# Kernel optimization log

Measured on AMD Instinct MI355X. Metric: run time of the kernel, lower is better.

The kernel has to match this reference:

```python
import jax, jax.numpy as jnp
import numpy as np

N, D, H, C, E, ED, HID = 50000, 160, 5, 32, 800000, 16, 512
EPS = 1e-5  # torch LayerNorm default
NEG_SLOPE = 0.2  # GATv2Conv default negative_slope


def layer_norm(x, g, b):
    mu = x.mean(-1, keepdims=True)
    var = x.var(-1, keepdims=True)  # biased, matches torch LayerNorm
    return (x - mu) * jax.lax.rsqrt(var + EPS) * g + b


def setup_inputs() -> dict:
    key = jax.random.key(0)
    ks = jax.random.split(key, 12)
    p = lambda k, shape: jax.random.normal(k, shape, jnp.float32) * 0.05
    z = lambda *s: jnp.zeros(s, jnp.float32)
    o = lambda *s: jnp.ones(s, jnp.float32)
    return {
        "x": jax.random.normal(ks[0], (N, D), jnp.float32),
        "edge_index": jax.random.randint(ks[1], (2, E), 0, N),
        "edge_attr": jax.random.normal(ks[2], (E, ED), jnp.float32),
        "u": jax.random.normal(ks[3], (1024, 64), jnp.float32),
        "batch": jax.random.randint(ks[4], (N,), 0, 1024),
        # GATv2Conv params (lin_l, lin_r, lin_edge, att, bias)
        "Wl": p(ks[5], (D, H * C)), "bl": z(H * C),
        "Wr": p(ks[6], (D, H * C)), "br": z(H * C),
        "We": p(ks[7], (ED, H * C)),
        "att": p(ks[8], (H, C)),
        "b_gat": z(H * C),
        # norm1
        "g1": o(D), "b1": z(D),
        # output MLP: Linear(D,HID) -> SELU -> LayerNorm(HID) -> Linear(HID,D)
        "W_m1": p(ks[9], (D, HID)), "b_m1": z(HID),
        "g_m": o(HID), "b_m": z(HID),
        "W_m2": p(ks[10], (HID, D)), "b_m2": z(D),
        # norm2
        "g2": o(D), "b2": z(D),
    }


def reference(x, edge_index, edge_attr, u, batch, Wl, bl, Wr, br, We, att, b_gat,
              g1, b1, W_m1, b_m1, g_m, b_m, W_m2, b_m2, g2, b2):
    src, dst = edge_index[0], edge_index[1]  # messages flow src -> dst
    xl = (x @ Wl + bl).reshape(N, H, C)      # source projection
    xr = (x @ Wr + br).reshape(N, H, C)      # target projection
    ea = (edge_attr @ We).reshape(E, H, C)
    # GATv2 scoring: att . leaky_relu(x_l[j] + x_r[i] + e_ij)
    e = jax.nn.leaky_relu(xl[src] + xr[dst] + ea, NEG_SLOPE)   # [E,H,C]
    score = jnp.einsum('ehc,hc->eh', e, att)                   # [E,H]
    # segment softmax over incoming edges of each target node
    mx = jax.ops.segment_max(score, dst, num_segments=N)       # [N,H]
    ex = jnp.exp(score - mx[dst])
    denom = jax.ops.segment_sum(ex, dst, num_segments=N)
    alpha = ex / denom[dst]                                    # [E,H]
    agg = jax.ops.segment_sum(alpha[:, :, None] * xl[src], dst, num_segments=N)
    attn = agg.reshape(N, H * C) + b_gat                       # concat heads
    # residual + norm, MLP, residual + norm (dropout=0)
    out = layer_norm(x + attn, g1, b1)
    h = layer_norm(jax.nn.selu(out @ W_m1 + b_m1), g_m, b_m)
    mlp = h @ W_m2 + b_m2
    return layer_norm(out + mlp, g2, b2)
```

## Files before the change

### kernel.cpp

```cpp
#include <hip/hip_runtime.h>
#include <math.h>

#define N_NODES 50000
#define D 160
#define H 5
#define C 32
#define HC 160
#define E_EDGES 800000
#define ED 16
#define HID 512
#define EPS 1e-5f
#define NEG_SLOPE 0.2f

typedef __attribute__((ext_vector_type(8))) short bf16x8;
typedef __attribute__((ext_vector_type(4))) float f32x4;
typedef __attribute__((ext_vector_type(4))) short short4v;

__device__ inline float bf2f(short s) {
  unsigned u = ((unsigned)(unsigned short)s) << 16;
  return __builtin_bit_cast(float, u);
}
__device__ inline short f2bf(float f) {
  unsigned u = __builtin_bit_cast(unsigned, f);
  u = u + 0x7fffu + ((u >> 16) & 1u);
  return (short)(u >> 16);
}
__device__ inline float selu_f(float v) {
  return 1.0507009873554805f * (v > 0.f ? v : 1.6732632423543772f * (__expf(v) - 1.f));
}

__global__ void prep_weights(const float* __restrict__ Wl, const float* __restrict__ Wr,
                             const float* __restrict__ Wm1, const float* __restrict__ Wm2,
                             const float* __restrict__ We,
                             short* __restrict__ WlT, short* __restrict__ WrT,
                             short* __restrict__ W1T, short* __restrict__ W2T,
                             short* __restrict__ WeTp) {
  int i = blockIdx.x * blockDim.x + threadIdx.x;
  if (i < 25600) { int n = i / 160, k = i % 160; WlT[n*160 + k] = f2bf(Wl[k*160 + n]); return; }
  i -= 25600;
  if (i < 25600) { int n = i / 160, k = i % 160; WrT[n*160 + k] = f2bf(Wr[k*160 + n]); return; }
  i -= 25600;
  if (i < 81920) { int n = i / 160, k = i % 160; W1T[n*160 + k] = f2bf(Wm1[k*512 + n]); return; }
  i -= 81920;
  if (i < 81920) { int n = i / 512, k = i % 512; W2T[n*512 + k] = f2bf(Wm2[k*160 + n]); return; }
  i -= 81920;
  if (i < 5120) { int col = i / 32, k = i % 32;
    WeTp[col*32 + k] = (k < ED) ? f2bf(We[k*160 + col]) : (short)0; }
}

__global__ void convert_x(const float* __restrict__ x, short* __restrict__ xb) {
  int i = blockIdx.x * blockDim.x + threadIdx.x;
  if (i < N_NODES * D / 8) {
    const float4* s = (const float4*)(x + (size_t)i * 8);
    float4 a = s[0], b = s[1];
    bf16x8 o;
    o[0] = f2bf(a.x); o[1] = f2bf(a.y); o[2] = f2bf(a.z); o[3] = f2bf(a.w);
    o[4] = f2bf(b.x); o[5] = f2bf(b.y); o[6] = f2bf(b.z); o[7] = f2bf(b.w);
    *(bf16x8*)(xb + (size_t)i * 8) = o;
  }
}

__global__ __launch_bounds__(256) void proj_mfma(
    const short* __restrict__ xb, const short* __restrict__ WlT, const short* __restrict__ WrT,
    const float* __restrict__ bl, const float* __restrict__ br,
    short* __restrict__ xl, short* __restrict__ xr)
{
  __shared__ short As[64][40];
  int t = threadIdx.x;
  int wave = t >> 6, lane = t & 63;
  int lq = lane >> 4, lc = lane & 15;
  int row0 = blockIdx.x * 64;
  f32x4 accl[10] = {}, accr[10] = {};
  for (int kt = 0; kt < 5; ++kt) {
    int k0 = kt * 32;
    {
      int r = t >> 2, seg = t & 3;
      int gr = min(row0 + r, N_NODES - 1);
      bf16x8 v = *(const bf16x8*)&xb[(size_t)gr * 160 + k0 + seg * 8];
      *(bf16x8*)&As[r][seg * 8] = v;
    }
    __syncthreads();
    bf16x8 af = *(bf16x8*)&As[wave * 16 + lc][lq * 8];
#pragma unroll
    for (int ct = 0; ct < 10; ++ct) {
      int cc = ct * 16 + lc;
      bf16x8 bfl = *(const bf16x8*)&WlT[cc * 160 + k0 + lq * 8];
      accl[ct] = __builtin_amdgcn_mfma_f32_16x16x32_bf16(af, bfl, accl[ct], 0, 0, 0);
      bf16x8 bfr = *(const bf16x8*)&WrT[cc * 160 + k0 + lq * 8];
      accr[ct] = __builtin_amdgcn_mfma_f32_16x16x32_bf16(af, bfr, accr[ct], 0, 0, 0);
    }
    __syncthreads();
  }
#pragma unroll
  for (int ct = 0; ct < 10; ++ct) {
    int col = ct * 16 + lc;
    float bbl = bl[col], bbr = br[col];
#pragma unroll
    for (int rg = 0; rg < 4; ++rg) {
      int row = row0 + wave * 16 + lq * 4 + rg;
      if (row < N_NODES) {
        xl[(size_t)row * 160 + col] = f2bf(accl[ct][rg] + bbl);
        xr[(size_t)row * 160 + col] = f2bf(accr[ct][rg] + bbr);
      }
    }
  }
}

__global__ void count_kernel(const int* __restrict__ ei, int* __restrict__ cnt) {
  int e = blockIdx.x * blockDim.x + threadIdx.x;
  if (e < E_EDGES) atomicAdd(&cnt[ei[E_EDGES + e]], 1);
}

__global__ __launch_bounds__(1024) void scan_kernel(const int* __restrict__ cnt,
                                                    int* __restrict__ offs) {
  const int PER = (N_NODES + 1023) / 1024;
  int t = threadIdx.x;
  int start = t * PER;
  int sum = 0;
  for (int i = 0; i < PER; ++i) {
    int idx = start + i;
    if (idx < N_NODES) sum += cnt[idx];
  }
  int lane = t & 63, wid = t >> 6;
  int v = sum;
  for (int off = 1; off < 64; off <<= 1) {
    int u = __shfl_up(v, off, 64);
    if (lane >= off) v += u;
  }
  __shared__ int wsums[16];
  if (lane == 63) wsums[wid] = v;
  __syncthreads();
  if (wid == 0) {
    int w = (lane < 16) ? wsums[lane] : 0;
    for (int off = 1; off < 16; off <<= 1) {
      int u = __shfl_up(w, off, 64);
      if (lane >= off) w += u;
    }
    if (lane < 16) wsums[lane] = w;
  }
  __syncthreads();
  int excl = v - sum + (wid > 0 ? wsums[wid - 1] : 0);
  int run = excl;
  for (int i = 0; i < PER; ++i) {
    int idx = start + i;
    if (idx < N_NODES) { offs[idx] = run; run += cnt[idx]; }
  }
  if (t == 1023) offs[N_NODES] = run;
}

__global__ void scatter3(const int* __restrict__ ei, const float* __restrict__ eattr,
                         const int* __restrict__ offs, int* __restrict__ cursor,
                         int* __restrict__ srcm, short* __restrict__ eacsr) {
  int e = blockIdx.x * blockDim.x + threadIdx.x;
  if (e < E_EDGES) {
    int dst = ei[E_EDGES + e];
    int src = ei[e];
    int slot = atomicAdd(&cursor[dst], 1);
    int j = offs[dst] + slot;
    srcm[j] = src * 160;
    const float4* s = (const float4*)&eattr[(size_t)e * ED];
    float4 v0 = s[0], v1 = s[1], v2 = s[2], v3 = s[3];
    short* o = eacsr + (size_t)j * ED;
    short4v w0, w1, w2, w3;
    w0[0]=f2bf(v0.x); w0[1]=f2bf(v0.y); w0[2]=f2bf(v0.z); w0[3]=f2bf(v0.w);
    w1[0]=f2bf(v1.x); w1[1]=f2bf(v1.y); w1[2]=f2bf(v1.z); w1[3]=f2bf(v1.w);
    w2[0]=f2bf(v2.x); w2[1]=f2bf(v2.y); w2[2]=f2bf(v2.z); w2[3]=f2bf(v2.w);
    w3[0]=f2bf(v3.x); w3[1]=f2bf(v3.y); w3[2]=f2bf(v3.z); w3[3]=f2bf(v3.w);
    *(short4v*)(o + 0) = w0; *(short4v*)(o + 4) = w1;
    *(short4v*)(o + 8) = w2; *(short4v*)(o + 12) = w3;
  }
}

__global__ __launch_bounds__(256) void attn_fused(
    const short* __restrict__ eacsr, const int* __restrict__ srcm,
    const short* __restrict__ WeTp, const short* __restrict__ xl, const short* __restrict__ xr,
    const float* __restrict__ att, const float* __restrict__ x,
    const float* __restrict__ b_gat, const float* __restrict__ g1, const float* __restrict__ b1,
    const int* __restrict__ offs,
    float* __restrict__ outb, short* __restrict__ outb_bf)
{
  int t = threadIdx.x;
  int wave = t >> 6, lane = t & 63;
  int lq = lane >> 4, lc = lane & 15;
  int i = blockIdx.x * 4 + wave;
  int e0 = offs[i], e1 = offs[i + 1];

  float xrv[10], attv[10];
#pragma unroll
  for (int ct = 0; ct < 10; ++ct) {
    xrv[ct] = bf2f(xr[(size_t)i * 160 + ct * 16 + lc]);
    attv[ct] = att[ct * 16 + lc];
  }
  float aggc[10] = {};
  float den[5] = {};
  const f32x4 zero4 = {};

  for (int j0 = e0; j0 < e1; j0 += 16) {
    bf16x8 af = {};
    if (lq < 2) {
      int jr = min(j0 + lc, e1 - 1);
      af = *(const bf16x8*)&eacsr[(size_t)jr * ED + lq * 8];
    }
    f32x4 acc[10];
#pragma unroll
    for (int ct = 0; ct < 10; ++ct) {
      bf16x8 bfv = *(const bf16x8*)&WeTp[(ct * 16 + lc) * 32 + lq * 8];
      acc[ct] = __builtin_amdgcn_mfma_f32_16x16x32_bf16(af, bfv, zero4, 0, 0, 0);
    }
    int src[4]; bool ok[4];
#pragma unroll
    for (int rg = 0; rg < 4; ++rg) {
      int j = j0 + lq * 4 + rg;
      ok[rg] = (j < e1);
      src[rg] = srcm[min(j, e1 - 1)];
    }
    float xlv[10][4];
    float partial[5][4] = {};
#pragma unroll
    for (int ct = 0; ct < 10; ++ct) {
#pragma unroll
      for (int rg = 0; rg < 4; ++rg) {
        float v = bf2f(xl[src[rg] + ct * 16 + lc]);
        xlv[ct][rg] = v;
        float z = acc[ct][rg] + v + xrv[ct];
        z = fmaxf(z, NEG_SLOPE * z);
        partial[ct >> 1][rg] = fmaf(z, attv[ct], partial[ct >> 1][rg]);
      }
    }
#pragma unroll
    for (int hh = 0; hh < 5; ++hh) {
#pragma unroll
      for (int rg = 0; rg < 4; ++rg) {
        float p = partial[hh][rg];
        p += __shfl_xor(p, 1, 64);
        p += __shfl_xor(p, 2, 64);
        p += __shfl_xor(p, 4, 64);
        p += __shfl_xor(p, 8, 64);
        float ex = ok[rg] ? __expf(p) : 0.f;
        den[hh] += ex;
        partial[hh][rg] = ex;
      }
    }
#pragma unroll
    for (int ct = 0; ct < 10; ++ct)
#pragma unroll
      for (int rg = 0; rg < 4; ++rg)
        aggc[ct] = fmaf(partial[ct >> 1][rg], xlv[ct][rg], aggc[ct]);
  }
#pragma unroll
  for (int ct = 0; ct < 10; ++ct) {
    aggc[ct] += __shfl_xor(aggc[ct], 16, 64);
    aggc[ct] += __shfl_xor(aggc[ct], 32, 64);
  }
#pragma unroll
  for (int hh = 0; hh < 5; ++hh) {
    den[hh] += __shfl_xor(den[hh], 16, 64);
    den[hh] += __shfl_xor(den[hh], 32, 64);
  }
  float val[10];
  float s1 = 0.f, s2 = 0.f;
#pragma unroll
  for (int ct = 0; ct < 10; ++ct) {
    float d = den[ct >> 1];
    float attn = (d > 0.f) ? aggc[ct] / d : 0.f;
    float v = x[(size_t)i * 160 + ct * 16 + lc] + attn + b_gat[ct * 16 + lc];
    val[ct] = v;
    s1 += v; s2 += v * v;
  }
#pragma unroll
  for (int m = 1; m <= 8; m <<= 1) { s1 += __shfl_xor(s1, m, 64); s2 += __shfl_xor(s2, m, 64); }
  float mu = s1 * (1.f / 160.f);
  float var = s2 * (1.f / 160.f) - mu * mu;
  float rstd = rsqrtf(var + EPS);
  if (lq == 0) {
#pragma unroll
    for (int ct = 0; ct < 10; ++ct) {
      int col = ct * 16 + lc;
      float o = (val[ct] - mu) * rstd * g1[col] + b1[col];
      outb[(size_t)i * 160 + col] = o;
      outb_bf[(size_t)i * 160 + col] = f2bf(o);
    }
  }
}

__global__ __launch_bounds__(256) void mlp1_mfma(
    const short* __restrict__ ab, const short* __restrict__ W1T,
    const float* __restrict__ b1m, const float* __restrict__ gm, const float* __restrict__ bm,
    short* __restrict__ h)
{
  __shared__ short As[32][40];
  __shared__ float ps1[4][32], ps2[4][32];
  int t = threadIdx.x;
  int wave = t >> 6, lane = t & 63;
  int lq = lane >> 4, lc = lane & 15;
  int row0 = blockIdx.x * 32;
  f32x4 acc[2][8] = {};
  for (int kt = 0; kt < 5; ++kt) {
    int k0 = kt * 32;
    if (t < 128) {
      int r = t >> 2, seg = t & 3;
      int gr = min(row0 + r, N_NODES - 1);
      bf16x8 v = *(const bf16x8*)&ab[(size_t)gr * 160 + k0 + seg * 8];
      *(bf16x8*)&As[r][seg * 8] = v;
    }
    __syncthreads();
    bf16x8 af0 = *(bf16x8*)&As[lc][lq * 8];
    bf16x8 af1 = *(bf16x8*)&As[16 + lc][lq * 8];
#pragma unroll
    for (int ct = 0; ct < 8; ++ct) {
      int cc = wave * 128 + ct * 16 + lc;
      bf16x8 bfv = *(const bf16x8*)&W1T[cc * 160 + k0 + lq * 8];
      acc[0][ct] = __builtin_amdgcn_mfma_f32_16x16x32_bf16(af0, bfv, acc[0][ct], 0, 0, 0);
      acc[1][ct] = __builtin_amdgcn_mfma_f32_16x16x32_bf16(af1, bfv, acc[1][ct], 0, 0, 0);
    }
    __syncthreads();
  }
  float s1[2][4] = {}, s2[2][4] = {};
#pragma unroll
  for (int rt = 0; rt < 2; ++rt)
#pragma unroll
    for (int ct = 0; ct < 8; ++ct)
#pragma unroll
      for (int rg = 0; rg < 4; ++rg) {
        int cc = wave * 128 + ct * 16 + lc;
        float v = selu_f(acc[rt][ct][rg] + b1m[cc]);
        acc[rt][ct][rg] = v;
        s1[rt][rg] += v; s2[rt][rg] += v * v;
      }
#pragma unroll
  for (int m = 1; m <= 8; m <<= 1) {
#pragma unroll
    for (int rt = 0; rt < 2; ++rt)
#pragma unroll
      for (int rg = 0; rg < 4; ++rg) {
        s1[rt][rg] += __shfl_xor(s1[rt][rg], m, 64);
        s2[rt][rg] += __shfl_xor(s2[rt][rg], m, 64);
      }
  }
  if (lc == 0) {
#pragma unroll
    for (int rt = 0; rt < 2; ++rt)
#pragma unroll
      for (int rg = 0; rg < 4; ++rg) {
        ps1[wave][rt * 16 + lq * 4 + rg] = s1[rt][rg];
        ps2[wave][rt * 16 + lq * 4 + rg] = s2[rt][rg];
      }
  }
  __syncthreads();
  float mu[2][4], rstd[2][4];
#pragma unroll
  for (int rt = 0; rt < 2; ++rt)
#pragma unroll
    for (int rg = 0; rg < 4; ++rg) {
      int rl = rt * 16 + lq * 4 + rg;
      float a = ps1[0][rl] + ps1[1][rl] + ps1[2][rl] + ps1[3][rl];
      float b = ps2[0][rl] + ps2[1][rl] + ps2[2][rl] + ps2[3][rl];
      float m_ = a * (1.f / 512.f);
      float var = b * (1.f / 512.f) - m_ * m_;
      mu[rt][rg] = m_; rstd[rt][rg] = rsqrtf(var + EPS);
    }
#pragma unroll
  for (int rt = 0; rt < 2; ++rt)
#pragma unroll
    for (int ct = 0; ct < 8; ++ct)
#pragma unroll
      for (int rg = 0; rg < 4; ++rg) {
        int row = row0 + rt * 16 + lq * 4 + rg;
        int cc = wave * 128 + ct * 16 + lc;
        if (row < N_NODES)
          h[(size_t)row * 512 + cc] =
              f2bf((acc[rt][ct][rg] - mu[rt][rg]) * rstd[rt][rg] * gm[cc] + bm[cc]);
      }
}

__global__ __launch_bounds__(256) void mlp2_mfma(
    const short* __restrict__ hb, const short* __restrict__ W2T,
    const float* __restrict__ b2m, const float* __restrict__ outb,
    const float* __restrict__ g2, const float* __restrict__ b2,
    float* __restrict__ y)
{
  __shared__ short As[128][72];
  int t = threadIdx.x;
  int wave = t >> 6, lane = t & 63;
  int lq = lane >> 4, lc = lane & 15;
  int row0 = blockIdx.x * 128;
  f32x4 acc[2][10] = {};
  for (int kt = 0; kt < 8; ++kt) {
    int k0 = kt * 64;
    __syncthreads();
#pragma unroll
    for (int q = 0; q < 4; ++q) {
      int idx = t + 256 * q;
      int r = idx >> 3, seg = idx & 7;
      int gr = min(row0 + r, N_NODES - 1);
      *(bf16x8*)&As[r][seg * 8] = *(const bf16x8*)&hb[(size_t)gr * 512 + k0 + seg * 8];
    }
    __syncthreads();
#pragma unroll
    for (int ks = 0; ks < 2; ++ks) {
      bf16x8 af0 = *(bf16x8*)&As[wave * 32 + lc][ks * 32 + lq * 8];
      bf16x8 af1 = *(bf16x8*)&As[wave * 32 + 16 + lc][ks * 32 + lq * 8];
#pragma unroll
      for (int ct = 0; ct < 10; ++ct) {
        bf16x8 bfv = *(const bf16x8*)&W2T[(ct * 16 + lc) * 512 + k0 + ks * 32 + lq * 8];
        acc[0][ct] = __builtin_amdgcn_mfma_f32_16x16x32_bf16(af0, bfv, acc[0][ct], 0, 0, 0);
        acc[1][ct] = __builtin_amdgcn_mfma_f32_16x16x32_bf16(af1, bfv, acc[1][ct], 0, 0, 0);
      }
    }
  }
  float s1[2][4] = {}, s2[2][4] = {};
#pragma unroll
  for (int rt = 0; rt < 2; ++rt)
#pragma unroll
    for (int ct = 0; ct < 10; ++ct) {
      int col = ct * 16 + lc;
#pragma unroll
      for (int rg = 0; rg < 4; ++rg) {
        int rowl = min(row0 + wave * 32 + rt * 16 + lq * 4 + rg, N_NODES - 1);
        float v = acc[rt][ct][rg] + b2m[col] + outb[(size_t)rowl * 160 + col];
        acc[rt][ct][rg] = v;
        s1[rt][rg] += v; s2[rt][rg] += v * v;
      }
    }
#pragma unroll
  for (int m = 1; m <= 8; m <<= 1) {
#pragma unroll
    for (int rt = 0; rt < 2; ++rt)
#pragma unroll
      for (int rg = 0; rg < 4; ++rg) {
        s1[rt][rg] += __shfl_xor(s1[rt][rg], m, 64);
        s2[rt][rg] += __shfl_xor(s2[rt][rg], m, 64);
      }
  }
  float mu[2][4], rstd[2][4];
#pragma unroll
  for (int rt = 0; rt < 2; ++rt)
#pragma unroll
    for (int rg = 0; rg < 4; ++rg) {
      float m_ = s1[rt][rg] * (1.f / 160.f);
      float var = s2[rt][rg] * (1.f / 160.f) - m_ * m_;
      mu[rt][rg] = m_; rstd[rt][rg] = rsqrtf(var + EPS);
    }
#pragma unroll
  for (int rt = 0; rt < 2; ++rt)
#pragma unroll
    for (int ct = 0; ct < 10; ++ct) {
      int col = ct * 16 + lc;
#pragma unroll
      for (int rg = 0; rg < 4; ++rg) {
        int row = row0 + wave * 32 + rt * 16 + lq * 4 + rg;
        if (row < N_NODES)
          y[(size_t)row * 160 + col] = (acc[rt][ct][rg] - mu[rt][rg]) * rstd[rt][rg] * g2[col] + b2[col];
      }
    }
}

extern "C" void kernel_launch(void* const* d_in, const int* in_sizes, int n_in,
                              void* d_out, int out_size, void* d_ws, size_t ws_size,
                              hipStream_t stream) {
  const float* x     = (const float*)d_in[0];
  const int*   ei    = (const int*)d_in[1];
  const float* eattr = (const float*)d_in[2];
  const float* Wl    = (const float*)d_in[5];
  const float* bl    = (const float*)d_in[6];
  const float* Wr    = (const float*)d_in[7];
  const float* br    = (const float*)d_in[8];
  const float* We    = (const float*)d_in[9];
  const float* att   = (const float*)d_in[10];
  const float* bgat  = (const float*)d_in[11];
  const float* g1    = (const float*)d_in[12];
  const float* b1    = (const float*)d_in[13];
  const float* Wm1   = (const float*)d_in[14];
  const float* bm1   = (const float*)d_in[15];
  const float* gm    = (const float*)d_in[16];
  const float* bm    = (const float*)d_in[17];
  const float* Wm2   = (const float*)d_in[18];
  const float* bm2   = (const float*)d_in[19];
  const float* g2    = (const float*)d_in[20];
  const float* b2    = (const float*)d_in[21];
  float* y = (float*)d_out;

  char* p = (char*)d_ws;
  auto alloc = [&](size_t bytes) {
    void* q = p;
    p += (bytes + 255) & ~(size_t)255;
    return q;
  };
  short* xb      = (short*)alloc((size_t)N_NODES * 160 * 2);
  short* xlb     = (short*)alloc((size_t)N_NODES * 160 * 2);
  short* xrb     = (short*)alloc((size_t)N_NODES * 160 * 2);
  float* outb    = (float*)alloc((size_t)N_NODES * 160 * 4);
  short* outb_bf = (short*)alloc((size_t)N_NODES * 160 * 2);
  short* hb      = (short*)alloc((size_t)N_NODES * 512 * 2);
  short* eacsr   = (short*)alloc((size_t)E_EDGES * ED * 2);
  int*   srcm    = (int*)alloc((size_t)E_EDGES * 4);
  short* WlT     = (short*)alloc(160 * 160 * 2);
  short* WrT     = (short*)alloc(160 * 160 * 2);
  short* W1T     = (short*)alloc(512 * 160 * 2);
  short* W2T     = (short*)alloc(160 * 512 * 2);
  short* WeTp    = (short*)alloc(160 * 32 * 2);
  int*   cnt     = (int*)alloc((size_t)N_NODES * 4);
  int*   offs    = (int*)alloc((size_t)(N_NODES + 1) * 4);
  int*   cursor  = (int*)alloc((size_t)N_NODES * 4);

  hipMemsetAsync(cnt, 0, (size_t)N_NODES * 4, stream);
  hipMemsetAsync(cursor, 0, (size_t)N_NODES * 4, stream);

  prep_weights<<<(220160 + 255) / 256, 256, 0, stream>>>(Wl, Wr, Wm1, Wm2, We,
                                                         WlT, WrT, W1T, W2T, WeTp);
  convert_x<<<(N_NODES * 160 / 8 + 255) / 256, 256, 0, stream>>>(x, xb);
  count_kernel<<<(E_EDGES + 255) / 256, 256, 0, stream>>>(ei, cnt);
  scan_kernel<<<1, 1024, 0, stream>>>(cnt, offs);
  scatter3<<<(E_EDGES + 255) / 256, 256, 0, stream>>>(ei, eattr, offs, cursor, srcm, eacsr);
  proj_mfma<<<(N_NODES + 63) / 64, 256, 0, stream>>>(xb, WlT, WrT, bl, br, xlb, xrb);
  attn_fused<<<N_NODES / 4, 256, 0, stream>>>(eacsr, srcm, WeTp, xlb, xrb, att, x,
                                              bgat, g1, b1, offs, outb, outb_bf);
  mlp1_mfma<<<(N_NODES + 31) / 32, 256, 0, stream>>>(outb_bf, W1T, bm1, gm, bm, hb);
  mlp2_mfma<<<(N_NODES + 127) / 128, 256, 0, stream>>>(hb, W2T, bm2, outb, g2, b2, y);
}
```

Measured before the change: 783.3 us.

## Stage gathered source rows in LDS and parallelize CSR offset scan

Replaces the single-block prefix scan over node in-degrees with a three-kernel multi-block scan (per-block scan, block-sum scan, add offsets). In the attention kernel, each wave now cooperatively gathers the 16 source xl rows for an edge chunk with 16-byte vector loads into padded shared memory, instead of each lane doing scattered 2-byte global loads. The MFMA edge projection is split into two halves to cut register pressure. The change adds LDS use and two extra launches; the LDS writes and reads within a wave rely on wave-level execution order with no explicit barrier.

Result: faster. 677.2 us (-13.5%).

```diff
diff --git a/kernel.cpp b/kernel.cpp
--- a/kernel.cpp
+++ b/kernel.cpp
@@ -111,41 +111,55 @@
   if (e < E_EDGES) atomicAdd(&cnt[ei[E_EDGES + e]], 1);
 }
 
-__global__ __launch_bounds__(1024) void scan_kernel(const int* __restrict__ cnt,
-                                                    int* __restrict__ offs) {
-  const int PER = (N_NODES + 1023) / 1024;
-  int t = threadIdx.x;
-  int start = t * PER;
-  int sum = 0;
-  for (int i = 0; i < PER; ++i) {
-    int idx = start + i;
-    if (idx < N_NODES) sum += cnt[idx];
-  }
+__global__ __launch_bounds__(1024) void scanA(const int* __restrict__ cnt,
+                                              int* __restrict__ pinc, int* __restrict__ bsum) {
+  int b = blockIdx.x, t = threadIdx.x;
+  int i = b * 1024 + t;
+  int v = (i < N_NODES) ? cnt[i] : 0;
   int lane = t & 63, wid = t >> 6;
-  int v = sum;
+  int s = v;
+#pragma unroll
   for (int off = 1; off < 64; off <<= 1) {
-    int u = __shfl_up(v, off, 64);
-    if (lane >= off) v += u;
-  }
-  __shared__ int wsums[16];
-  if (lane == 63) wsums[wid] = v;
+    int u = __shfl_up(s, off, 64);
+    if (lane >= off) s += u;
+  }
+  __shared__ int ws[16];
+  if (lane == 63) ws[wid] = s;
   __syncthreads();
   if (wid == 0) {
-    int w = (lane < 16) ? wsums[lane] : 0;
+    int w = (lane < 16) ? ws[lane] : 0;
+#pragma unroll
     for (int off = 1; off < 16; off <<= 1) {
       int u = __shfl_up(w, off, 64);
       if (lane >= off) w += u;
     }
-    if (lane < 16) wsums[lane] = w;
+    if (lane < 16) ws[lane] = w;
   }
   __syncthreads();
-  int excl = v - sum + (wid > 0 ? wsums[wid - 1] : 0);
-  int run = excl;
-  for (int i = 0; i < PER; ++i) {
-    int idx = start + i;
-    if (idx < N_NODES) { offs[idx] = run; run += cnt[idx]; }
-  }
-  if (t == 1023) offs[N_NODES] = run;
+  int incl = s + (wid > 0 ? ws[wid - 1] : 0);
+  if (i < N_NODES) pinc[i] = incl;
+  if (t == 1023) bsum[b] = incl;
+}
+
+__global__ void scanB(const int* __restrict__ bsum, int* __restrict__ boff) {
+  int t = threadIdx.x;
+  int v = (t < 49) ? bsum[t] : 0;
+  int s = v;
+#pragma unroll
+  for (int off = 1; off < 64; off <<= 1) {
+    int u = __shfl_up(s, off, 64);
+    if (t >= off) s += u;
+  }
+  if (t < 49) boff[t] = s - v;
+}
+
+__global__ __launch_bounds__(1024) void scanC(const int* __restrict__ pinc,
+                                              const int* __restrict__ boff,
+                                              int* __restrict__ offs) {
+  int b = blockIdx.x, t = threadIdx.x;
+  int i = b * 1024 + t;
+  if (i < N_NODES) offs[i + 1] = pinc[i] + boff[b];
+  if (i == 0) offs[0] = 0;
 }
 
 __global__ void scatter3(const int* __restrict__ ei, const float* __restrict__ eattr,
@@ -179,52 +193,68 @@
     const int* __restrict__ offs,
     float* __restrict__ outb, short* __restrict__ outb_bf)
 {
+  __shared__ short xt[4][16][168];
   int t = threadIdx.x;
   int wave = t >> 6, lane = t & 63;
   int lq = lane >> 4, lc = lane & 15;
   int i = blockIdx.x * 4 + wave;
   int e0 = offs[i], e1 = offs[i + 1];
-
-  float xrv[10], attv[10];
-#pragma unroll
-  for (int ct = 0; ct < 10; ++ct) {
-    xrv[ct] = bf2f(xr[(size_t)i * 160 + ct * 16 + lc]);
-    attv[ct] = att[ct * 16 + lc];
-  }
+  short* myt = &xt[wave][0][0];
+
+  int segE[5], segS[5];
+#pragma unroll
+  for (int p = 0; p < 5; ++p) {
+    int g = p * 64 + lane;
+    int e = (g * 3277) >> 16;
+    segE[p] = e;
+    segS[p] = g - e * 20;
+  }
+
   float aggc[10] = {};
   float den[5] = {};
   const f32x4 zero4 = {};
 
   for (int j0 = e0; j0 < e1; j0 += 16) {
+#pragma unroll
+    for (int p = 0; p < 5; ++p) {
+      int j = j0 + segE[p];
+      if (j > e1 - 1) j = e1 - 1;
+      int srow = srcm[j];
+      bf16x8 v = *(const bf16x8*)&xl[(size_t)srow + segS[p] * 8];
+      *(bf16x8*)&myt[segE[p] * 168 + segS[p] * 8] = v;
+    }
     bf16x8 af = {};
     if (lq < 2) {
       int jr = min(j0 + lc, e1 - 1);
       af = *(const bf16x8*)&eacsr[(size_t)jr * ED + lq * 8];
     }
-    f32x4 acc[10];
-#pragma unroll
-    for (int ct = 0; ct < 10; ++ct) {
-      bf16x8 bfv = *(const bf16x8*)&WeTp[(ct * 16 + lc) * 32 + lq * 8];
-      acc[ct] = __builtin_amdgcn_mfma_f32_16x16x32_bf16(af, bfv, zero4, 0, 0, 0);
-    }
-    int src[4]; bool ok[4];
-#pragma unroll
-    for (int rg = 0; rg < 4; ++rg) {
-      int j = j0 + lq * 4 + rg;
-      ok[rg] = (j < e1);
-      src[rg] = srcm[min(j, e1 - 1)];
-    }
-    float xlv[10][4];
+    bool ok[4];
+#pragma unroll
+    for (int rg = 0; rg < 4; ++rg) ok[rg] = (j0 + lq * 4 + rg) < e1;
+
     float partial[5][4] = {};
 #pragma unroll
-    for (int ct = 0; ct < 10; ++ct) {
-#pragma unroll
-      for (int rg = 0; rg < 4; ++rg) {
-        float v = bf2f(xl[src[rg] + ct * 16 + lc]);
-        xlv[ct][rg] = v;
-        float z = acc[ct][rg] + v + xrv[ct];
-        z = fmaxf(z, NEG_SLOPE * z);
-        partial[ct >> 1][rg] = fmaf(z, attv[ct], partial[ct >> 1][rg]);
+    for (int half = 0; half < 2; ++half) {
+      f32x4 acc[5];
+#pragma unroll
+      for (int cs = 0; cs < 5; ++cs) {
+        int ct = half * 5 + cs;
+        bf16x8 bfv = *(const bf16x8*)&WeTp[(ct * 16 + lc) * 32 + lq * 8];
+        acc[cs] = __builtin_amdgcn_mfma_f32_16x16x32_bf16(af, bfv, zero4, 0, 0, 0);
+      }
+#pragma unroll
+      for (int cs = 0; cs < 5; ++cs) {
+        int ct = half * 5 + cs;
+        int col = ct * 16 + lc;
+        float attv = att[col];
+        float xrv = bf2f(xr[(size_t)i * 160 + col]);
+#pragma unroll
+        for (int rg = 0; rg < 4; ++rg) {
+          float xlv = bf2f(myt[(lq * 4 + rg) * 168 + col]);
+          float z = acc[cs][rg] + xlv + xrv;
+          z = fmaxf(z, NEG_SLOPE * z);
+          partial[ct >> 1][rg] = fmaf(z, attv, partial[ct >> 1][rg]);
+        }
       }
     }
 #pragma unroll
@@ -242,10 +272,14 @@
       }
     }
 #pragma unroll
-    for (int ct = 0; ct < 10; ++ct)
-#pragma unroll
-      for (int rg = 0; rg < 4; ++rg)
-        aggc[ct] = fmaf(partial[ct >> 1][rg], xlv[ct][rg], aggc[ct]);
+    for (int ct = 0; ct < 10; ++ct) {
+      int col = ct * 16 + lc;
+#pragma unroll
+      for (int rg = 0; rg < 4; ++rg) {
+        float xlv = bf2f(myt[(lq * 4 + rg) * 168 + col]);
+        aggc[ct] = fmaf(partial[ct >> 1][rg], xlv, aggc[ct]);
+      }
+    }
   }
 #pragma unroll
   for (int ct = 0; ct < 10; ++ct) {
@@ -502,6 +536,9 @@
   int*   cnt     = (int*)alloc((size_t)N_NODES * 4);
   int*   offs    = (int*)alloc((size_t)(N_NODES + 1) * 4);
   int*   cursor  = (int*)alloc((size_t)N_NODES * 4);
+  int*   pinc    = (int*)alloc((size_t)N_NODES * 4);
+  int*   bsum    = (int*)alloc(64 * 4);
+  int*   boff    = (int*)alloc(64 * 4);
 
   hipMemsetAsync(cnt, 0, (size_t)N_NODES * 4, stream);
   hipMemsetAsync(cursor, 0, (size_t)N_NODES * 4, stream);
@@ -510,7 +547,9 @@
                                                          WlT, WrT, W1T, W2T, WeTp);
   convert_x<<<(N_NODES * 160 / 8 + 255) / 256, 256, 0, stream>>>(x, xb);
   count_kernel<<<(E_EDGES + 255) / 256, 256, 0, stream>>>(ei, cnt);
-  scan_kernel<<<1, 1024, 0, stream>>>(cnt, offs);
+  scanA<<<49, 1024, 0, stream>>>(cnt, pinc, bsum);
+  scanB<<<1, 64, 0, stream>>>(bsum, boff);
+  scanC<<<49, 1024, 0, stream>>>(pinc, boff, offs);
   scatter3<<<(E_EDGES + 255) / 256, 256, 0, stream>>>(ei, eattr, offs, cursor, srcm, eacsr);
   proj_mfma<<<(N_NODES + 63) / 64, 256, 0, stream>>>(xb, WlT, WrT, bl, br, xlb, xrb);
   attn_fused<<<N_NODES / 4, 256, 0, stream>>>(eacsr, srcm, WeTp, xlb, xrb, att, x,
```
